# Optimization experiments

Hardware: AMD Instinct MI355X
Metric: run time of the kernel (lower is better)

The kernel has to match this reference:

```python
import jax, jax.numpy as jnp
import numpy as np
import math

EMBED_DIM = 2048
NUM_HEADS = 16
HEAD_DIM = EMBED_DIM // NUM_HEADS
BATCH = 2
SEQ = 2048


def setup_inputs() -> dict:
    key = jax.random.key(0)
    ks = jax.random.split(key, 6)
    x = jax.random.normal(ks[0], (BATCH, SEQ, EMBED_DIM), dtype=jnp.float32)
    # causal mask: True = masked (upper triangle, strictly above diagonal)
    attn_mask = jnp.triu(jnp.ones((SEQ, SEQ), dtype=bool), k=1)
    s = 1.0 / math.sqrt(EMBED_DIM)
    W_qkv = jax.random.normal(ks[1], (3 * EMBED_DIM, EMBED_DIM), dtype=jnp.float32) * s
    b_qkv = jax.random.normal(ks[2], (3 * EMBED_DIM,), dtype=jnp.float32) * 0.01
    W_out = jax.random.normal(ks[3], (EMBED_DIM, EMBED_DIM), dtype=jnp.float32) * s
    b_out = jax.random.normal(ks[4], (EMBED_DIM,), dtype=jnp.float32) * 0.01
    return {"x": x, "W_qkv": W_qkv, "b_qkv": b_qkv, "W_out": W_out,
            "b_out": b_out, "attn_mask": attn_mask}


def reference(x, W_qkv, b_qkv, W_out, b_out, attn_mask):
    B, S, E = x.shape
    # fused QKV projection: [B,S,3E]
    qkv = jnp.einsum('bse,fe->bsf', x, W_qkv) + b_qkv
    qkv = qkv.reshape(B, S, 3, NUM_HEADS, HEAD_DIM)
    qkv = jnp.transpose(qkv, (2, 0, 3, 1, 4))  # [3,B,H,S,Dh]
    q, k, v = qkv[0], qkv[1], qkv[2]
    scale = 1.0 / math.sqrt(HEAD_DIM)
    scores = jnp.einsum('bhqd,bhkd->bhqk', q, k) * scale  # [B,H,S,S]
    scores = jnp.where(attn_mask[None, None, :, :], -jnp.inf, scores)
    attn = jax.nn.softmax(scores, axis=-1)
    out = jnp.einsum('bhqk,bhkd->bhqd', attn, v)  # [B,H,S,Dh]
    out = jnp.transpose(out, (0, 2, 1, 3)).reshape(B, S, E)
    out = jnp.einsum('bse,fe->bsf', out, W_out) + b_out
    return out
```

## Files before the change

kernel.cpp:

```cpp
#include <hip/hip_runtime.h>
#include <hip/hip_bf16.h>
#include <math.h>

#define SEQ   2048
#define EMBED 2048
#define NHEAD 16
#define DHEAD 128
#define BATCH 2

#define NX   ((size_t)BATCH * SEQ * EMBED)
#define NW1  ((size_t)3 * EMBED * EMBED)
#define NB1  ((size_t)3 * EMBED)
#define NW2  ((size_t)EMBED * EMBED)
#define NB2  ((size_t)EMBED)

typedef __bf16 bf16;
typedef __attribute__((__ext_vector_type__(8))) __bf16 bf16x8;
typedef __attribute__((__ext_vector_type__(4))) __bf16 bf16x4;
typedef __attribute__((__ext_vector_type__(4))) float f32x4;
typedef __attribute__((__ext_vector_type__(4))) unsigned int u32x4;

#define NEG_BIG (-1.0e30f)

__device__ __forceinline__ f32x4 mfma_16x16x32(bf16x8 a, bf16x8 b, f32x4 c) {
  return __builtin_amdgcn_mfma_f32_16x16x32_bf16(a, b, c, 0, 0, 0);
}

__device__ __forceinline__ void llds16(bf16* dst, const bf16* src) {
  __builtin_amdgcn_global_load_lds(
      (const __attribute__((address_space(1))) void*)src,
      (__attribute__((address_space(3))) void*)dst, 16, 0, 0);
}

#define BARRAW() asm volatile("s_barrier" ::: "memory")

__global__ void convert_inputs(const void* __restrict__ xin,
                               const void* __restrict__ w1in,
                               const void* __restrict__ b1in,
                               const void* __restrict__ w2in,
                               const void* __restrict__ b2in,
                               bf16* __restrict__ xb, bf16* __restrict__ w1b,
                               bf16* __restrict__ b1b, bf16* __restrict__ w2b,
                               bf16* __restrict__ b2b, int* __restrict__ flagp)
{
  __shared__ int sflag;
  if (threadIdx.x == 0) sflag = 0;
  __syncthreads();
  const unsigned short* xh = (const unsigned short*)xin;
  int huge = 0;
  for (int i = threadIdx.x; i < 2048; i += 256) {
    float f = __uint_as_float((unsigned int)xh[i] << 16);
    if (!(fabsf(f) <= 1e4f)) huge = 1;
  }
  if (huge) sflag = 1;
  __syncthreads();
  const int isf32 = sflag;
  if (blockIdx.x == 0 && threadIdx.x == 0) *flagp = isf32;

  const void* srcs[5] = {xin, w1in, b1in, w2in, b2in};
  bf16* dsts[5] = {xb, w1b, b1b, w2b, b2b};
  const size_t lens[5] = {NX, NW1, NB1, NW2, NB2};
  const size_t gid = (size_t)blockIdx.x * blockDim.x + threadIdx.x;
  const size_t gstride = (size_t)gridDim.x * blockDim.x;
  for (int sidx = 0; sidx < 5; ++sidx) {
    const size_t n8 = lens[sidx] >> 3;
    bf16* d = dsts[sidx];
    if (isf32) {
      const float* s = (const float*)srcs[sidx];
      for (size_t i = gid; i < n8; i += gstride) {
        const float* sp = s + i * 8;
        bf16x8 r;
#pragma unroll
        for (int j = 0; j < 8; ++j) r[j] = (bf16)sp[j];
        *(bf16x8*)(d + i * 8) = r;
      }
    } else {
      const u32x4* s = (const u32x4*)srcs[sidx];
      for (size_t i = gid; i < n8; i += gstride)
        *(u32x4*)(d + i * 8) = s[i];
    }
  }
}

template <int MODE>
__global__ __launch_bounds__(512, 1) void gemmE(
    const bf16* __restrict__ A, const bf16* __restrict__ B,
    const bf16* __restrict__ bias, int K,
    void* __restrict__ out0v, bf16* __restrict__ out1, bf16* __restrict__ out2,
    const int* __restrict__ flagp)
{
  __shared__ __align__(16) bf16 lds_[49152];
  constexpr int NTX = (MODE == 0) ? 24 : 8;
  const int t = threadIdx.x;
  const int lane = t & 63, w = t >> 6;
  const int wm = w >> 2, wn = w & 3;
  const int lr = lane & 15, lq = lane >> 4;
  const int nwg = 32 * NTX;
  const int f = blockIdx.x;
  const int o = (f & 7) * (nwg >> 3) + (f >> 3);
  const int by = o & 31, bx = o >> 5;
  const int m0 = by << 7, n0 = bx << 8;
  const int NT = K >> 6;
  const int NI = NT >> 1;

  const int srow = t >> 2;
  const int sg8 = (((t & 3) ^ (((t >> 5) & 1) << 1))) << 3;

#define STAGE3(kt_, ks_)                                                     \
  {                                                                          \
    const int _kt = (kt_), _ks = (ks_);                                      \
    if (_kt < NT) {                                                          \
      const int _bb = (_kt & 1) * 24576;                                     \
      const int _kc = (_kt << 6) + _ks * 32;                                 \
      llds16(lds_ + _bb + _ks * 4096 + (w << 9),                             \
             A + (size_t)(m0 + srow) * K + _kc + sg8);                       \
      llds16(lds_ + _bb + 8192 + _ks * 8192 + (w << 9),                      \
             B + (size_t)(n0 + srow) * K + _kc + sg8);                       \
      llds16(lds_ + _bb + 8192 + _ks * 8192 + 4096 + (w << 9),               \
             B + (size_t)(n0 + 128 + srow) * K + _kc + sg8);                 \
    }                                                                        \
  }

  f32x4 acc[4][4];
#pragma unroll
  for (int i = 0; i < 4; ++i)
#pragma unroll
    for (int j = 0; j < 4; ++j) acc[i][j] = (f32x4){0.f, 0.f, 0.f, 0.f};

  const int rg8 = ((lq ^ (((lr >> 3) & 1) << 1))) << 3;
  const int arow = (wm * 64 + lr) * 32 + rg8;
  const int brow = (wn * 64 + lr) * 32 + rg8;

  STAGE3(0, 0);
  STAGE3(0, 1);
  STAGE3(1, 0);
  asm volatile("s_waitcnt vmcnt(6)" ::: "memory");
  BARRAW();

  for (int i = 0; i < NI; ++i) {
    const int k2 = i << 1;
#pragma unroll
    for (int p = 0; p < 4; ++p) {
      const int ks = p & 1;
      const int bufb = (p >> 1) * 24576;
      bf16x8 af[4], bfv[4];
      const int ab = bufb + ks * 4096 + arow;
      const int bb = bufb + 8192 + ks * 8192 + brow;
#pragma unroll
      for (int mi = 0; mi < 4; ++mi)
        af[mi] = *(const bf16x8*)(lds_ + ab + mi * 512);
#pragma unroll
      for (int ni = 0; ni < 4; ++ni)
        bfv[ni] = *(const bf16x8*)(lds_ + bb + ni * 512);
      if (p == 0)      STAGE3(k2 + 1, 1)
      else if (p == 1) STAGE3(k2 + 2, 0)
      else if (p == 2) STAGE3(k2 + 2, 1)
      else             STAGE3(k2 + 3, 0)
      BARRAW();
      __builtin_amdgcn_s_setprio(1);
#pragma unroll
      for (int mi = 0; mi < 4; ++mi)
#pragma unroll
        for (int ni = 0; ni < 4; ++ni)
          acc[mi][ni] = mfma_16x16x32(af[mi], bfv[ni], acc[mi][ni]);
      __builtin_amdgcn_s_setprio(0);
      if (i == 0 && p == 0) {
        asm volatile("s_waitcnt vmcnt(6)" ::: "memory");
      }
      if (p == 1) {
        if (i == NI - 1) { asm volatile("s_waitcnt vmcnt(0)" ::: "memory"); }
        else             { asm volatile("s_waitcnt vmcnt(3)" ::: "memory"); }
      }
      if (p == 3 && i < NI - 1) {
        asm volatile("s_waitcnt vmcnt(3)" ::: "memory");
      }
      BARRAW();
    }
  }
#undef STAGE3

  if (MODE == 0) {
    const int which = n0 >> 11;
    const int bbid = m0 >> 11;
    const int s0 = m0 & 2047;
    if (which == 2) {
      bf16* dst = out2;
#pragma unroll
      for (int ni = 0; ni < 4; ++ni) {
        const int ng = n0 + wn * 64 + ni * 16 + lr;
        const int h = (ng >> 7) & 15;
        const int d = ng & 127;
        const float bv = (float)bias[ng];
        bf16* rowp =
            dst + ((size_t)(bbid * NHEAD + h) * DHEAD + d) * SEQ + s0 + wm * 64;
#pragma unroll
        for (int mi = 0; mi < 4; ++mi) {
          bf16x4 pk;
#pragma unroll
          for (int reg = 0; reg < 4; ++reg)
            pk[reg] = (bf16)(acc[mi][ni][reg] + bv);
          *(bf16x4*)(rowp + mi * 16 + lq * 4) = pk;
        }
      }
    } else {
      bf16* dst = (which == 0) ? (bf16*)out0v : out1;
#pragma unroll
      for (int ni = 0; ni < 4; ++ni) {
        const int ng = n0 + wn * 64 + ni * 16 + lr;
        const int h = (ng >> 7) & 15;
        const int d = ng & 127;
        const float bv = (float)bias[ng];
        bf16* hb = dst + (size_t)(bbid * NHEAD + h) * SEQ * DHEAD + d;
#pragma unroll
        for (int mi = 0; mi < 4; ++mi)
#pragma unroll
          for (int reg = 0; reg < 4; ++reg) {
            const int s = s0 + wm * 64 + mi * 16 + lq * 4 + reg;
            hb[(size_t)s * DHEAD] = (bf16)(acc[mi][ni][reg] + bv);
          }
      }
    }
  } else {
    const int isf32 = *flagp;
#pragma unroll
    for (int ni = 0; ni < 4; ++ni) {
      const int col = n0 + wn * 64 + ni * 16 + lr;
      const float bv = (float)bias[col];
#pragma unroll
      for (int mi = 0; mi < 4; ++mi)
#pragma unroll
        for (int reg = 0; reg < 4; ++reg) {
          const int row = m0 + wm * 64 + mi * 16 + lq * 4 + reg;
          const float v = acc[mi][ni][reg] + bv;
          const size_t idx = (size_t)row * EMBED + col;
          if (isf32) ((float*)out0v)[idx] = v;
          else       ((bf16*)out0v)[idx] = (bf16)v;
        }
    }
  }
}

__device__ __forceinline__ void qk_softmax_tile(
    const bf16* __restrict__ sK, bf16* __restrict__ sP, const bf16x8* aq,
    float& m_i, float& l_i, f32x4* oacc, int kt, int qt,
    int w, int lr, int lq, int sPofs)
{
  const float scale = 0.08838834764831845f;
  f32x4 tacc[4];
#pragma unroll
  for (int ni = 0; ni < 4; ++ni) tacc[ni] = (f32x4){0.f, 0.f, 0.f, 0.f};
#pragma unroll
  for (int ks = 0; ks < 4; ++ks)
#pragma unroll
    for (int ni = 0; ni < 4; ++ni) {
      bf16x8 bk = *(const bf16x8*)(sK + (ni * 16 + lr) * 136 + ks * 32 + lq * 8);
      tacc[ni] = mfma_16x16x32(bk, aq[ks], tacc[ni]);
    }
  float pp[4][4];
  const int qg = qt * 64 + w * 16 + lr;
#pragma unroll
  for (int ni = 0; ni < 4; ++ni)
#pragma unroll
    for (int reg = 0; reg < 4; ++reg) {
      float sv = tacc[ni][reg] * scale;
      if (kt == qt) {
        const int kg = kt * 64 + ni * 16 + lq * 4 + reg;
        if (kg > qg) sv = NEG_BIG;
      }
      pp[ni][reg] = sv;
    }
  float mx;
  {
    float a0 = fmaxf(fmaxf(pp[0][0], pp[0][1]), fmaxf(pp[0][2], pp[0][3]));
    float a1 = fmaxf(fmaxf(pp[1][0], pp[1][1]), fmaxf(pp[1][2], pp[1][3]));
    float a2 = fmaxf(fmaxf(pp[2][0], pp[2][1]), fmaxf(pp[2][2], pp[2][3]));
    float a3 = fmaxf(fmaxf(pp[3][0], pp[3][1]), fmaxf(pp[3][2], pp[3][3]));
    mx = fmaxf(fmaxf(a0, a1), fmaxf(a2, a3));
  }
  mx = fmaxf(mx, __shfl_xor(mx, 16, 64));
  mx = fmaxf(mx, __shfl_xor(mx, 32, 64));
  const float mnew = fmaxf(m_i, mx);
  const float alpha = __expf(m_i - mnew);
  float ls = 0.f;
#pragma unroll
  for (int ni = 0; ni < 4; ++ni) {
    float s0 = __expf(pp[ni][0] - mnew);
    float s1 = __expf(pp[ni][1] - mnew);
    float s2 = __expf(pp[ni][2] - mnew);
    float s3 = __expf(pp[ni][3] - mnew);
    pp[ni][0] = s0; pp[ni][1] = s1; pp[ni][2] = s2; pp[ni][3] = s3;
    ls += (s0 + s1) + (s2 + s3);
  }
  ls += __shfl_xor(ls, 16, 64);
  ls += __shfl_xor(ls, 32, 64);
  l_i = l_i * alpha + ls;
  m_i = mnew;
#pragma unroll
  for (int dt = 0; dt < 8; ++dt) oacc[dt] *= alpha;
  bf16* rowp = sP + (sPofs + w * 16 + lr) * 64;
  const int swz = lr & 7;
#pragma unroll
  for (int ni = 0; ni < 4; ++ni) {
    bf16x4 pk;
#pragma unroll
    for (int reg = 0; reg < 4; ++reg) pk[reg] = (bf16)pp[ni][reg];
    const int col = ni * 16 + lq * 4;
    const int scol = (((col >> 3) ^ swz) << 3) | (col & 7);
    *(bf16x4*)(rowp + scol) = pk;
  }
}

__device__ __forceinline__ void pv_tile(const bf16* __restrict__ sP,
                                        const bf16* __restrict__ sV,
                                        f32x4* oacc, int w, int lr, int lq,
                                        int sPofs)
{
  const bf16* rowp = sP + (sPofs + w * 16 + lr) * 64;
  const int swz = lr & 7;
#pragma unroll
  for (int ks2 = 0; ks2 < 2; ++ks2) {
    const int chunk = ks2 * 4 + lq;
    bf16x8 bp = *(const bf16x8*)(rowp + ((chunk ^ swz) << 3));
#pragma unroll
    for (int dt = 0; dt < 8; ++dt) {
      bf16x8 av =
          *(const bf16x8*)(sV + (dt * 16 + lr) * 72 + ks2 * 32 + lq * 8);
      oacc[dt] = mfma_16x16x32(av, bp, oacc[dt]);
    }
  }
}

__global__ __launch_bounds__(256, 2) void attn_fwd(
    const bf16* __restrict__ qb, const bf16* __restrict__ kb,
    const bf16* __restrict__ vt, bf16* __restrict__ aout)
{
  __shared__ bf16 sK[64 * 136];
  __shared__ bf16 sV[128 * 72];
  __shared__ bf16 sP[128 * 64];
  const int t = threadIdx.x;
  const int lane = t & 63, w = t >> 6;
  const int lr = lane & 15, lq = lane >> 4;
  const int p  = blockIdx.x & 15;
  const int bh = blockIdx.x >> 4;
  const int bb = bh >> 4, h = bh & 15;
  const int qlo = p, qhi = 31 - p;

  bf16x8 aqL[4], aqH[4];
  {
    const bf16* qpL =
        qb + ((size_t)bh * SEQ + qlo * 64 + w * 16 + lr) * DHEAD + lq * 8;
    const bf16* qpH =
        qb + ((size_t)bh * SEQ + qhi * 64 + w * 16 + lr) * DHEAD + lq * 8;
#pragma unroll
    for (int ks = 0; ks < 4; ++ks) {
      aqL[ks] = *(const bf16x8*)(qpL + ks * 32);
      aqH[ks] = *(const bf16x8*)(qpH + ks * 32);
    }
  }

  f32x4 oL[8], oH[8];
#pragma unroll
  for (int i = 0; i < 8; ++i) {
    oL[i] = (f32x4){0.f, 0.f, 0.f, 0.f};
    oH[i] = (f32x4){0.f, 0.f, 0.f, 0.f};
  }
  float mL = NEG_BIG, mH = NEG_BIG;
  float lL = 0.f, lH = 0.f;

  bf16x8 rk[4], rv[4];
  const int kr_ = t >> 4, kd_ = t & 15;
  const int vr_ = t >> 3, vk_ = t & 7;
#define FETCH(ktv)                                                          \
  {                                                                         \
    const int _kt = (ktv);                                                  \
    _Pragma("unroll") for (int i = 0; i < 4; ++i) {                         \
      rk[i] = *(const bf16x8*)(kb + ((size_t)bh * SEQ + _kt * 64 +          \
                                     (i * 16 + kr_)) * DHEAD + kd_ * 8);    \
      rv[i] = *(const bf16x8*)(vt + ((size_t)bh * DHEAD + (i * 32 + vr_)) * \
                                     SEQ + _kt * 64 + vk_ * 8);             \
    }                                                                       \
  }
#define COMMIT()                                                            \
  {                                                                         \
    _Pragma("unroll") for (int i = 0; i < 4; ++i) {                         \
      *(bf16x8*)(sK + (i * 16 + kr_) * 136 + kd_ * 8) = rk[i];              \
      *(bf16x8*)(sV + (i * 32 + vr_) * 72 + vk_ * 8) = rv[i];               \
    }                                                                       \
  }

  FETCH(0);
  COMMIT();
  __syncthreads();

  for (int kt = 0; kt <= qhi; ++kt) {
    if (kt < qhi) FETCH(kt + 1);
    const bool doLo = (kt <= qlo);

    qk_softmax_tile(sK, sP, aqH, mH, lH, oH, kt, qhi, w, lr, lq, 64);
    if (doLo) qk_softmax_tile(sK, sP, aqL, mL, lL, oL, kt, qlo, w, lr, lq, 0);
    asm volatile("s_waitcnt lgkmcnt(0)" ::: "memory");
    pv_tile(sP, sV, oH, w, lr, lq, 64);
    if (doLo) pv_tile(sP, sV, oL, w, lr, lq, 0);

    __syncthreads();
    if (kt < qhi) {
      COMMIT();
      __syncthreads();
    }
  }

#pragma unroll
  for (int side = 0; side < 2; ++side) {
    const f32x4* oacc = side ? oH : oL;
    const float linv = 1.0f / (side ? lH : lL);
    const int qt = side ? qhi : qlo;
    const int qg = qt * 64 + w * 16 + lr;
    bf16* outp = aout + ((size_t)bb * SEQ + qg) * EMBED + h * 128 + lq * 4;
#pragma unroll
    for (int dt = 0; dt < 8; ++dt) {
      bf16x4 pk;
#pragma unroll
      for (int reg = 0; reg < 4; ++reg)
        pk[reg] = (bf16)(oacc[dt][reg] * linv);
      *(bf16x4*)(outp + dt * 16) = pk;
    }
  }
#undef FETCH
#undef COMMIT
}

extern "C" void kernel_launch(void* const* d_in, const int* in_sizes, int n_in,
                              void* d_out, int out_size, void* d_ws, size_t ws_size,
                              hipStream_t stream) {
  const void* x    = d_in[0];
  const void* Wqkv = d_in[1];
  const void* bqkv = d_in[2];
  const void* Wout = d_in[3];
  const void* bout = d_in[4];

  int* flagp = (int*)d_ws;
  bf16* base = (bf16*)((char*)d_ws + 256);
  bf16* xb   = base;
  bf16* w1b  = xb + NX;
  bf16* b1b  = w1b + NW1;
  bf16* w2b  = b1b + NB1;
  bf16* b2b  = w2b + NW2;
  bf16* qb   = b2b + NB2;
  bf16* kb   = qb + NX;
  bf16* vt   = kb + NX;
  bf16* aout = vt + NX;

  convert_inputs<<<dim3(1024), dim3(256), 0, stream>>>(
      x, Wqkv, bqkv, Wout, bout, xb, w1b, b1b, w2b, b2b, flagp);
  gemmE<0><<<dim3(768), dim3(512), 0, stream>>>(
      xb, w1b, b1b, EMBED, (void*)qb, kb, vt, flagp);
  attn_fwd<<<dim3(512), dim3(256), 0, stream>>>(qb, kb, vt, aout);
  gemmE<1><<<dim3(256), dim3(512), 0, stream>>>(
      aout, w2b, b2b, EMBED, d_out, nullptr, nullptr, flagp);
}
```

Baseline: 395.0 us.

## Replace QKV projection GEMM with 256x256-tile double-buffered kernel

```diff
diff --git a/kernel.cpp b/kernel.cpp
--- a/kernel.cpp
+++ b/kernel.cpp
@@ -78,6 +78,127 @@
       const u32x4* s = (const u32x4*)srcs[sidx];
       for (size_t i = gid; i < n8; i += gstride)
         *(u32x4*)(d + i * 8) = s[i];
+    }
+  }
+}
+
+__global__ __launch_bounds__(512, 1) void gemmM(
+    const bf16* __restrict__ A, const bf16* __restrict__ B,
+    const bf16* __restrict__ bias,
+    bf16* __restrict__ outq, bf16* __restrict__ outk, bf16* __restrict__ outv)
+{
+  __shared__ __align__(16) bf16 lds_[65536];
+  const int t = threadIdx.x;
+  const int lane = t & 63, w = t >> 6;
+  const int wm = w >> 2, wn = w & 3;
+  const int lr = lane & 15, lq = lane >> 4;
+  const int f = blockIdx.x;
+  const int o = (f & 7) * 48 + (f >> 3);
+  const int by = o & 15, bx = o >> 4;
+  const int m0 = by << 8, n0 = bx << 8;
+  const int K = EMBED;
+  const int NT = K >> 6;
+
+  const int sg8 = ((lane & 3) ^ (((lane >> 5) & 1) << 1)) << 3;
+  const bf16* aS  = A + (size_t)(m0 + w * 32 + (lane >> 2)) * K + sg8;
+  const bf16* aS2 = aS + (size_t)16 * K;
+  const bf16* bS  = B + (size_t)(n0 + w * 32 + (lane >> 2)) * K + sg8;
+  const bf16* bS2 = bS + (size_t)16 * K;
+  const int dA = w * 1024;
+  const int dB = 16384 + w * 1024;
+
+#define STAGE_HALF(kt_, ks_)                                                 \
+  {                                                                          \
+    const int _bufb = ((kt_) & 1) * 32768 + (ks_) * 8192;                    \
+    const int _kc = ((kt_) << 6) + (ks_) * 32;                               \
+    llds16(lds_ + _bufb + dA, aS + _kc);                                     \
+    llds16(lds_ + _bufb + dA + 512, aS2 + _kc);                              \
+    llds16(lds_ + _bufb + dB, bS + _kc);                                     \
+    llds16(lds_ + _bufb + dB + 512, bS2 + _kc);                              \
+  }
+
+  f32x4 acc[8][4];
+#pragma unroll
+  for (int i = 0; i < 8; ++i)
+#pragma unroll
+    for (int j = 0; j < 4; ++j) acc[i][j] = (f32x4){0.f, 0.f, 0.f, 0.f};
+
+  const int rg8 = (lq ^ (((lr >> 3) & 1) << 1)) << 3;
+  const int arow_ = (wm * 128 + lr) * 32 + rg8;
+  const int brow_ = 16384 + (wn * 64 + lr) * 32 + rg8;
+
+  STAGE_HALF(0, 0);
+  STAGE_HALF(0, 1);
+  asm volatile("s_waitcnt vmcnt(0)" ::: "memory");
+  BARRAW();
+
+  for (int tt = 0; tt < NT; ++tt) {
+    const int bufb = (tt & 1) * 32768;
+#pragma unroll
+    for (int ks = 0; ks < 2; ++ks) {
+      const int base = bufb + ks * 8192;
+      bf16x8 af[8], bfv[4];
+#pragma unroll
+      for (int ai = 0; ai < 8; ++ai)
+        af[ai] = *(const bf16x8*)(lds_ + base + arow_ + ai * 512);
+#pragma unroll
+      for (int ni = 0; ni < 4; ++ni)
+        bfv[ni] = *(const bf16x8*)(lds_ + base + brow_ + ni * 512);
+      if (tt + 1 < NT) STAGE_HALF(tt + 1, ks);
+      __builtin_amdgcn_s_setprio(1);
+#pragma unroll
+      for (int ai = 0; ai < 8; ++ai)
+#pragma unroll
+        for (int ni = 0; ni < 4; ++ni)
+          acc[ai][ni] = mfma_16x16x32(af[ai], bfv[ni], acc[ai][ni]);
+      __builtin_amdgcn_s_setprio(0);
+      if (tt + 1 < NT) {
+        asm volatile("s_waitcnt vmcnt(4)" ::: "memory");
+      } else if (ks == 0) {
+        asm volatile("s_waitcnt vmcnt(0)" ::: "memory");
+      }
+      BARRAW();
+    }
+  }
+#undef STAGE_HALF
+
+  const int which = n0 >> 11;
+  const int bbid = m0 >> 11;
+  const int s0 = m0 & 2047;
+  if (which == 2) {
+#pragma unroll
+    for (int ni = 0; ni < 4; ++ni) {
+      const int ng = n0 + wn * 64 + ni * 16 + lr;
+      const int h = (ng >> 7) & 15;
+      const int d = ng & 127;
+      const float bv = (float)bias[ng];
+      bf16* rowp =
+          outv + ((size_t)(bbid * NHEAD + h) * DHEAD + d) * SEQ + s0 + wm * 128;
+#pragma unroll
+      for (int ai = 0; ai < 8; ++ai) {
+        bf16x4 pk;
+#pragma unroll
+        for (int reg = 0; reg < 4; ++reg)
+          pk[reg] = (bf16)(acc[ai][ni][reg] + bv);
+        *(bf16x4*)(rowp + ai * 16 + lq * 4) = pk;
+      }
+    }
+  } else {
+    bf16* dst = (which == 0) ? outq : outk;
+#pragma unroll
+    for (int ni = 0; ni < 4; ++ni) {
+      const int ng = n0 + wn * 64 + ni * 16 + lr;
+      const int h = (ng >> 7) & 15;
+      const int d = ng & 127;
+      const float bv = (float)bias[ng];
+      bf16* hb = dst + (size_t)(bbid * NHEAD + h) * SEQ * DHEAD + d;
+#pragma unroll
+      for (int ai = 0; ai < 8; ++ai)
+#pragma unroll
+        for (int reg = 0; reg < 4; ++reg) {
+          const int s = s0 + wm * 128 + ai * 16 + lq * 4 + reg;
+          hb[(size_t)s * DHEAD] = (bf16)(acc[ai][ni][reg] + bv);
+        }
     }
   }
 }
@@ -452,8 +573,7 @@
 
   convert_inputs<<<dim3(1024), dim3(256), 0, stream>>>(
       x, Wqkv, bqkv, Wout, bout, xb, w1b, b1b, w2b, b2b, flagp);
-  gemmE<0><<<dim3(768), dim3(512), 0, stream>>>(
-      xb, w1b, b1b, EMBED, (void*)qb, kb, vt, flagp);
+  gemmM<<<dim3(384), dim3(512), 0, stream>>>(xb, w1b, b1b, qb, kb, vt);
   attn_fwd<<<dim3(512), dim3(256), 0, stream>>>(qb, kb, vt, aout);
   gemmE<1><<<dim3(256), dim3(512), 0, stream>>>(
       aout, w2b, b2b, EMBED, d_out, nullptr, nullptr, flagp);
```

Result: no change. 388.7 us (-1.6%).
